# Kernel optimization log

Hardware: AMD Instinct MI355X
Metric: run time of the kernel (lower is better)

The kernel has to match this reference:

```python
import jax, jax.numpy as jnp
import numpy as np

B, E, S = 8, 128, 4096


def setup_inputs() -> dict:
    key = jax.random.key(0)
    ks = jax.random.split(key, 7)
    sc = 1.0 / np.sqrt(E)
    return {
        "x": jax.random.normal(ks[0], (B, E, S), dtype=jnp.float32),
        "Wq": jax.random.normal(ks[1], (E, E), dtype=jnp.float32) * sc,
        "bq": jax.random.normal(ks[2], (E,), dtype=jnp.float32) * 0.01,
        "Wk": jax.random.normal(ks[3], (E, E), dtype=jnp.float32) * sc,
        "bk": jax.random.normal(ks[4], (E,), dtype=jnp.float32) * 0.01,
        "Wv": jax.random.normal(ks[5], (E, E), dtype=jnp.float32) * sc,
        "bv": jax.random.normal(ks[6], (E,), dtype=jnp.float32) * 0.01,
    }


def reference(x, Wq, bq, Wk, bk, Wv, bv):
    # x: [B, E, S]; Conv1d(k=1) == per-position linear over channels.
    # Project then move to [B, S, E] (matches .permute(0, 2, 1)).
    Q = jnp.einsum('bes,fe->bsf', x, Wq) + bq  # [B, S, E]
    K = jnp.einsum('bes,fe->bsf', x, Wk) + bk
    V = jnp.einsum('bes,fe->bsf', x, Wv) + bv
    scale = jnp.sqrt(jnp.asarray(float(x.shape[1]), dtype=jnp.float32))
    attn = jnp.einsum('bqe,bke->bqk', Q, K) / scale  # [B, S, S]
    attn = jax.nn.softmax(attn, axis=2)
    out = jnp.einsum('bqk,bke->bqe', attn, V)  # [B, S, E]
    return out.transpose(0, 2, 1)  # [B, E, S]
```

## Files before the change

kernel.cpp:

```cpp
#include <hip/hip_runtime.h>
#include <math.h>

#define NB 8
#define NE 128
#define NS 4096
#define CSCALE 0.12751743f

typedef short s8v __attribute__((ext_vector_type(8)));
typedef float f4v __attribute__((ext_vector_type(4)));
typedef float f16v __attribute__((ext_vector_type(16)));
typedef unsigned int u32;
typedef unsigned int u2v __attribute__((ext_vector_type(2)));
typedef __attribute__((address_space(1))) const u32* gp1_t;
typedef __attribute__((address_space(3))) u32* lp3_t;

__device__ __forceinline__ ushort f2bf(float f) {
  union { float f; unsigned u; } v; v.f = f;
  unsigned r = v.u + 0x7fffu + ((v.u >> 16) & 1u);
  return (ushort)(r >> 16);
}
__device__ __forceinline__ float bf2f(ushort h) {
  union { unsigned u; float f; } v; v.u = ((unsigned)h) << 16; return v.f;
}
__device__ __forceinline__ void gload_lds16(const void* g, void* l) {
  __builtin_amdgcn_global_load_lds((gp1_t)g, (lp3_t)l, 16, 0, 0);
}
__device__ __forceinline__ u32 cvtpk(float lo, float hi) {
  u32 r;
  asm("v_cvt_pk_bf16_f32 %0, %1, %2" : "=v"(r) : "v"(lo), "v"(hi));
  return r;
}
__device__ __forceinline__ void split8(const float* __restrict__ p, float scale,
                                       s8v& hi, s8v& lo) {
  union { s8v v; ushort u[8]; } H, L;
  #pragma unroll
  for (int i = 0; i < 8; ++i) {
    float v = p[i] * scale;
    ushort h = f2bf(v);
    H.u[i] = h;
    L.u[i] = f2bf(v - bf2f(h));
  }
  hi = H.v; lo = L.v;
}

__global__ __launch_bounds__(256, 2) void proj_gemm(
    const float* __restrict__ x,
    const float* __restrict__ Wq, const float* __restrict__ bq,
    const float* __restrict__ Wk, const float* __restrict__ bk,
    const float* __restrict__ Wv, const float* __restrict__ bv,
    ushort* __restrict__ Qn, ushort* __restrict__ Kn, ushort* __restrict__ Vt)
{
  const int tid = threadIdx.x;
  const int wv = tid >> 6, lane = tid & 63;
  const int g = lane >> 4, c = lane & 15;
  const int bid = blockIdx.x;
  const int b = bid & 7;
  const int s0 = (bid >> 3) * 64;
  const float* xb = x + (size_t)b * NE * NS;

  __shared__ __align__(16) ushort xh[64][136], xl[64][136];

  {
    const int ss = tid & 63, cq = tid >> 6;
    #pragma unroll
    for (int p = 0; p < 4; ++p) {
      const int ch = p * 4 + cq;
      union { s8v v; ushort u[8]; } H, L;
      #pragma unroll
      for (int i = 0; i < 8; ++i) {
        float v = xb[(size_t)(ch * 8 + i) * NS + s0 + ss];
        ushort hi = f2bf(v);
        H.u[i] = hi;
        L.u[i] = f2bf(v - bf2f(hi));
      }
      *(s8v*)&xh[ss][ch * 8] = H.v;
      *(s8v*)&xl[ss][ch * 8] = L.v;
    }
  }
  __syncthreads();

  f4v aq[2][4], ak[2][4], av[2][4];
  #pragma unroll
  for (int i = 0; i < 2; ++i)
    #pragma unroll
    for (int j = 0; j < 4; ++j) {
      aq[i][j] = (f4v){0.f,0.f,0.f,0.f};
      ak[i][j] = (f4v){0.f,0.f,0.f,0.f};
      av[i][j] = (f4v){0.f,0.f,0.f,0.f};
    }

  #pragma unroll
  for (int ks = 0; ks < 4; ++ks) {
    s8v xbh[4], xbl[4];
    #pragma unroll
    for (int st = 0; st < 4; ++st) {
      xbh[st] = *(const s8v*)&xh[st * 16 + c][ks * 32 + g * 8];
      xbl[st] = *(const s8v*)&xl[st * 16 + c][ks * 32 + g * 8];
    }
    #pragma unroll
    for (int ftl = 0; ftl < 2; ++ftl) {
      const int f0 = (wv * 2 + ftl) * 16;
      const size_t wo = (size_t)(f0 + c) * NE + ks * 32 + g * 8;
      s8v qh, ql, kh, kl, vh, vl;
      split8(Wq + wo, CSCALE, qh, ql);
      split8(Wk + wo, 1.0f,   kh, kl);
      split8(Wv + wo, 1.0f,   vh, vl);
      #pragma unroll
      for (int st = 0; st < 4; ++st) {
        aq[ftl][st] = __builtin_amdgcn_mfma_f32_16x16x32_bf16(xbh[st], qh, aq[ftl][st], 0, 0, 0);
        aq[ftl][st] = __builtin_amdgcn_mfma_f32_16x16x32_bf16(xbl[st], qh, aq[ftl][st], 0, 0, 0);
        aq[ftl][st] = __builtin_amdgcn_mfma_f32_16x16x32_bf16(xbh[st], ql, aq[ftl][st], 0, 0, 0);
        av[ftl][st] = __builtin_amdgcn_mfma_f32_16x16x32_bf16(vh, xbh[st], av[ftl][st], 0, 0, 0);
        av[ftl][st] = __builtin_amdgcn_mfma_f32_16x16x32_bf16(vh, xbl[st], av[ftl][st], 0, 0, 0);
        av[ftl][st] = __builtin_amdgcn_mfma_f32_16x16x32_bf16(vl, xbh[st], av[ftl][st], 0, 0, 0);
        ak[ftl][st] = __builtin_amdgcn_mfma_f32_16x16x32_bf16(xbh[st], kh, ak[ftl][st], 0, 0, 0);
        ak[ftl][st] = __builtin_amdgcn_mfma_f32_16x16x32_bf16(xbl[st], kh, ak[ftl][st], 0, 0, 0);
        ak[ftl][st] = __builtin_amdgcn_mfma_f32_16x16x32_bf16(xbh[st], kl, ak[ftl][st], 0, 0, 0);
      }
    }
  }

  ushort* Qnb = Qn + (size_t)b * NS * NE;
  ushort* Knb = Kn + (size_t)b * NS * NE;
  ushort* Vtb = Vt + (size_t)b * NE * NS;
  #pragma unroll
  for (int ftl = 0; ftl < 2; ++ftl) {
    const int f0 = (wv * 2 + ftl) * 16;
    #pragma unroll
    for (int r = 0; r < 4; ++r) {
      const int f = f0 + 4 * g + r;
      const float bvv = bv[f];
      #pragma unroll
      for (int st = 0; st < 4; ++st)
        Vtb[(size_t)f * NS + s0 + st * 16 + c] = f2bf(av[ftl][st][r] + bvv);
    }
    const float bqv = bq[f0 + c] * CSCALE;
    const float bkv = bk[f0 + c];
    #pragma unroll
    for (int st = 0; st < 4; ++st)
      #pragma unroll
      for (int r = 0; r < 4; ++r) {
        const size_t ro = (size_t)(s0 + st * 16 + 4 * g + r) * NE + f0 + c;
        Qnb[ro] = f2bf(aq[ftl][st][r] + bqv);
        Knb[ro] = f2bf(ak[ftl][st][r] + bkv);
      }
  }
}

__global__ __launch_bounds__(256) void attn_kernel(
    const ushort* __restrict__ Qn, const ushort* __restrict__ Kn,
    const ushort* __restrict__ Vt, float* __restrict__ out)
{
  const int tid = threadIdx.x;
  const int wv = tid >> 6, lane = tid & 63;
  const int h = lane >> 5, q5 = lane & 31;
  const int bid = blockIdx.x;
  const int b = bid & 7;
  const int qw = (bid >> 3) * 128 + wv * 32;

  const ushort* Qb = Qn + (size_t)b * NS * NE;
  const char*   Kb = (const char*)(Kn + (size_t)b * NS * NE);
  const char*   Vb = (const char*)(Vt + (size_t)b * NE * NS);

  __shared__ __align__(16) char ldsK[2][16384];
  __shared__ __align__(16) char ldsV[2][16384];

  s8v qf[8];
  #pragma unroll
  for (int dc = 0; dc < 8; ++dc)
    qf[dc] = *(const s8v*)(Qb + (size_t)(qw + q5) * NE + dc * 16 + h * 8);

  auto stage = [&](int buf, int kt) {
    const char* Ksrc = Kb + (size_t)kt * (64 * 256);
    #pragma unroll
    for (int p = 0; p < 4; ++p) {
      const int off = wv * 4096 + p * 1024;
      const int lo = off + lane * 16;
      const int row = lo >> 8;
      gload_lds16(Ksrc + (lo ^ ((row & 7) << 4)), &ldsK[buf][off]);
    }
    #pragma unroll
    for (int p = 0; p < 4; ++p) {
      const int off = wv * 4096 + p * 1024;
      const int lo = off + lane * 16;
      const int row = lo >> 7;
      const int inner = (lo & 127) ^ ((row & 7) << 4);
      gload_lds16(Vb + (size_t)row * (NS * 2) + kt * 128 + inner, &ldsV[buf][off]);
    }
  };

  f16v o[4];
  #pragma unroll
  for (int dt = 0; dt < 4; ++dt)
    o[dt] = (f16v){0,0,0,0,0,0,0,0,0,0,0,0,0,0,0,0};
  float lsum = 0.f;

  stage(0, 0);
  asm volatile("s_waitcnt vmcnt(0)" ::: "memory");
  __syncthreads();

  #pragma unroll 1
  for (int kt = 0; kt < NS / 64; ++kt) {
    const int cur = kt & 1;
    if (kt + 1 < NS / 64) stage(cur ^ 1, kt + 1);
    const char* bK = ldsK[cur];
    const char* bV = ldsV[cur];

    #pragma unroll
    for (int kc = 0; kc < 2; ++kc) {
      f16v s = (f16v){0,0,0,0,0,0,0,0,0,0,0,0,0,0,0,0};
      #pragma unroll
      for (int dc = 0; dc < 8; ++dc) {
        s8v kf = *(const s8v*)(bK + (kc * 32 + q5) * 256 + ((dc * 32 + h * 16) ^ ((q5 & 7) << 4)));
        s = __builtin_amdgcn_mfma_f32_32x32x16_bf16(kf, qf[dc], s, 0, 0, 0);
      }
      float p[16];
      #pragma unroll
      for (int r = 0; r < 16; ++r) {
        p[r] = __builtin_amdgcn_exp2f(s[r]);
        lsum += p[r];
      }
      #pragma unroll
      for (int ksl = 0; ksl < 2; ++ksl) {
        const int r0 = ksl * 8;
        u32 A = cvtpk(p[r0 + 0], p[r0 + 1]);
        u32 B = cvtpk(p[r0 + 4], p[r0 + 5]);
        u32 C = cvtpk(p[r0 + 2], p[r0 + 3]);
        u32 D = cvtpk(p[r0 + 6], p[r0 + 7]);
        u2v rAB = __builtin_amdgcn_permlane32_swap(A, B, false, false);
        u2v rCD = __builtin_amdgcn_permlane32_swap(C, D, false, false);
        union { s8v v; u32 w[4]; } P;
        P.w[0] = rAB[0]; P.w[1] = rCD[0]; P.w[2] = rAB[1]; P.w[3] = rCD[1];
        const int ks = kc * 2 + ksl;
        #pragma unroll
        for (int dt = 0; dt < 4; ++dt) {
          s8v vf = *(const s8v*)(bV + (dt * 32 + q5) * 128 + ((ks * 32 + h * 16) ^ ((q5 & 7) << 4)));
          o[dt] = __builtin_amdgcn_mfma_f32_32x32x16_bf16(vf, P.v, o[dt], 0, 0, 0);
        }
      }
    }
    asm volatile("s_waitcnt vmcnt(0)" ::: "memory");
    __syncthreads();
  }

  lsum += __shfl_xor(lsum, 32);
  const float rinv = 1.0f / lsum;
  float* ob = out + (size_t)b * NE * NS;
  #pragma unroll
  for (int dt = 0; dt < 4; ++dt)
    #pragma unroll
    for (int r = 0; r < 16; ++r) {
      const int e = dt * 32 + (r & 3) + 8 * (r >> 2) + 4 * h;
      ob[(size_t)e * NS + qw + q5] = o[dt][r] * rinv;
    }
}

extern "C" void kernel_launch(void* const* d_in, const int* in_sizes, int n_in,
                              void* d_out, int out_size, void* d_ws, size_t ws_size,
                              hipStream_t stream) {
  const float* x  = (const float*)d_in[0];
  const float* Wq = (const float*)d_in[1];
  const float* bq = (const float*)d_in[2];
  const float* Wk = (const float*)d_in[3];
  const float* bk = (const float*)d_in[4];
  const float* Wv = (const float*)d_in[5];
  const float* bv = (const float*)d_in[6];
  float* out = (float*)d_out;

  ushort* Qn = (ushort*)d_ws;
  ushort* Kn = Qn + (size_t)NB * NS * NE;
  ushort* Vt = Kn + (size_t)NB * NS * NE;

  proj_gemm<<<dim3(NS / 64 * NB), 256, 0, stream>>>(x, Wq, bq, Wk, bk, Wv, bv, Qn, Kn, Vt);
  attn_kernel<<<dim3(NS / 128 * NB), 256, 0, stream>>>(Qn, Kn, Vt, out);
}
```

Before: 118.0 us.

## Split KV range across wave pairs with two query tiles per wave

Each wave now handles two 32-row query tiles, so every K and V fragment read from LDS feeds two MFMAs. The four waves form two slices that each cover half of the key sequence with their own double-buffered LDS tiles. The partial outputs and row sums are then combined through LDS at the end. This halves LDS fragment reads per MFMA but doubles accumulator registers and LDS footprint (about 128KB), and adds a final cross-wave reduction; launch bounds now force one block per CU.

```diff
diff --git a/kernel.cpp b/kernel.cpp
--- a/kernel.cpp
+++ b/kernel.cpp
@@ -147,95 +147,111 @@
   }
 }
 
-__global__ __launch_bounds__(256) void attn_kernel(
+__global__ __launch_bounds__(256, 1) void attn_kernel(
     const ushort* __restrict__ Qn, const ushort* __restrict__ Kn,
     const ushort* __restrict__ Vt, float* __restrict__ out)
 {
   const int tid = threadIdx.x;
   const int wv = tid >> 6, lane = tid & 63;
   const int h = lane >> 5, q5 = lane & 31;
+  const int slice = wv >> 1;
+  const int ws = wv & 1;
   const int bid = blockIdx.x;
   const int b = bid & 7;
-  const int qw = (bid >> 3) * 128 + wv * 32;
+  const int qw = (bid >> 3) * 128 + ws * 64;
 
   const ushort* Qb = Qn + (size_t)b * NS * NE;
   const char*   Kb = (const char*)(Kn + (size_t)b * NS * NE);
   const char*   Vb = (const char*)(Vt + (size_t)b * NE * NS);
 
-  __shared__ __align__(16) char ldsK[2][16384];
-  __shared__ __align__(16) char ldsV[2][16384];
-
-  s8v qf[8];
-  #pragma unroll
-  for (int dc = 0; dc < 8; ++dc)
-    qf[dc] = *(const s8v*)(Qb + (size_t)(qw + q5) * NE + dc * 16 + h * 8);
-
-  auto stage = [&](int buf, int kt) {
+  __shared__ __align__(16) char ldsK[2][2][16384];
+  __shared__ __align__(16) char ldsV[2][2][16384];
+  __shared__ float lx[2][2][32];
+
+  s8v qf[2][8];
+  #pragma unroll
+  for (int u = 0; u < 2; ++u)
+    #pragma unroll
+    for (int dc = 0; dc < 8; ++dc)
+      qf[u][dc] = *(const s8v*)(Qb + (size_t)(qw + u * 32 + q5) * NE + dc * 16 + h * 8);
+
+  auto stage = [&](int buf, int t) {
+    const int kt = slice * 32 + t;
     const char* Ksrc = Kb + (size_t)kt * (64 * 256);
     #pragma unroll
-    for (int p = 0; p < 4; ++p) {
-      const int off = wv * 4096 + p * 1024;
+    for (int p = 0; p < 8; ++p) {
+      const int off = ws * 8192 + p * 1024;
       const int lo = off + lane * 16;
       const int row = lo >> 8;
-      gload_lds16(Ksrc + (lo ^ ((row & 7) << 4)), &ldsK[buf][off]);
-    }
-    #pragma unroll
-    for (int p = 0; p < 4; ++p) {
-      const int off = wv * 4096 + p * 1024;
+      gload_lds16(Ksrc + (lo ^ ((row & 15) << 4)), &ldsK[slice][buf][off]);
+    }
+    #pragma unroll
+    for (int p = 0; p < 8; ++p) {
+      const int off = ws * 8192 + p * 1024;
       const int lo = off + lane * 16;
       const int row = lo >> 7;
       const int inner = (lo & 127) ^ ((row & 7) << 4);
-      gload_lds16(Vb + (size_t)row * (NS * 2) + kt * 128 + inner, &ldsV[buf][off]);
+      gload_lds16(Vb + (size_t)row * (NS * 2) + kt * 128 + inner, &ldsV[slice][buf][off]);
     }
   };
 
-  f16v o[4];
-  #pragma unroll
-  for (int dt = 0; dt < 4; ++dt)
-    o[dt] = (f16v){0,0,0,0,0,0,0,0,0,0,0,0,0,0,0,0};
-  float lsum = 0.f;
+  auto makefrag = [&](const float* p, int r0) -> s8v {
+    u32 A = cvtpk(p[r0 + 0], p[r0 + 1]);
+    u32 B = cvtpk(p[r0 + 4], p[r0 + 5]);
+    u32 C = cvtpk(p[r0 + 2], p[r0 + 3]);
+    u32 D = cvtpk(p[r0 + 6], p[r0 + 7]);
+    u2v rAB = __builtin_amdgcn_permlane32_swap(A, B, false, false);
+    u2v rCD = __builtin_amdgcn_permlane32_swap(C, D, false, false);
+    union { s8v v; u32 w[4]; } P;
+    P.w[0] = rAB[0]; P.w[1] = rCD[0]; P.w[2] = rAB[1]; P.w[3] = rCD[1];
+    return P.v;
+  };
+
+  f16v oA[4], oB[4];
+  #pragma unroll
+  for (int dt = 0; dt < 4; ++dt) {
+    oA[dt] = (f16v){0,0,0,0,0,0,0,0,0,0,0,0,0,0,0,0};
+    oB[dt] = (f16v){0,0,0,0,0,0,0,0,0,0,0,0,0,0,0,0};
+  }
+  float lA = 0.f, lB = 0.f;
 
   stage(0, 0);
   asm volatile("s_waitcnt vmcnt(0)" ::: "memory");
   __syncthreads();
 
   #pragma unroll 1
-  for (int kt = 0; kt < NS / 64; ++kt) {
-    const int cur = kt & 1;
-    if (kt + 1 < NS / 64) stage(cur ^ 1, kt + 1);
-    const char* bK = ldsK[cur];
-    const char* bV = ldsV[cur];
+  for (int t = 0; t < 32; ++t) {
+    const int cur = t & 1;
+    if (t + 1 < 32) stage(cur ^ 1, t + 1);
+    const char* bK = ldsK[slice][cur];
+    const char* bV = ldsV[slice][cur];
 
     #pragma unroll
     for (int kc = 0; kc < 2; ++kc) {
-      f16v s = (f16v){0,0,0,0,0,0,0,0,0,0,0,0,0,0,0,0};
+      f16v sA = (f16v){0,0,0,0,0,0,0,0,0,0,0,0,0,0,0,0};
+      f16v sB = (f16v){0,0,0,0,0,0,0,0,0,0,0,0,0,0,0,0};
       #pragma unroll
       for (int dc = 0; dc < 8; ++dc) {
-        s8v kf = *(const s8v*)(bK + (kc * 32 + q5) * 256 + ((dc * 32 + h * 16) ^ ((q5 & 7) << 4)));
-        s = __builtin_amdgcn_mfma_f32_32x32x16_bf16(kf, qf[dc], s, 0, 0, 0);
-      }
-      float p[16];
+        s8v kf = *(const s8v*)(bK + (kc * 32 + q5) * 256 + ((dc * 32 + h * 16) ^ ((q5 & 15) << 4)));
+        sA = __builtin_amdgcn_mfma_f32_32x32x16_bf16(kf, qf[0][dc], sA, 0, 0, 0);
+        sB = __builtin_amdgcn_mfma_f32_32x32x16_bf16(kf, qf[1][dc], sB, 0, 0, 0);
+      }
+      float pA[16], pB[16];
       #pragma unroll
       for (int r = 0; r < 16; ++r) {
-        p[r] = __builtin_amdgcn_exp2f(s[r]);
-        lsum += p[r];
+        pA[r] = __builtin_amdgcn_exp2f(sA[r]); lA += pA[r];
+        pB[r] = __builtin_amdgcn_exp2f(sB[r]); lB += pB[r];
       }
       #pragma unroll
       for (int ksl = 0; ksl < 2; ++ksl) {
-        const int r0 = ksl * 8;
-        u32 A = cvtpk(p[r0 + 0], p[r0 + 1]);
-        u32 B = cvtpk(p[r0 + 4], p[r0 + 5]);
-        u32 C = cvtpk(p[r0 + 2], p[r0 + 3]);
-        u32 D = cvtpk(p[r0 + 6], p[r0 + 7]);
-        u2v rAB = __builtin_amdgcn_permlane32_swap(A, B, false, false);
-        u2v rCD = __builtin_amdgcn_permlane32_swap(C, D, false, false);
-        union { s8v v; u32 w[4]; } P;
-        P.w[0] = rAB[0]; P.w[1] = rCD[0]; P.w[2] = rAB[1]; P.w[3] = rCD[1];
+        s8v PA = makefrag(pA, ksl * 8);
+        s8v PB = makefrag(pB, ksl * 8);
         const int ks = kc * 2 + ksl;
         #pragma unroll
         for (int dt = 0; dt < 4; ++dt) {
           s8v vf = *(const s8v*)(bV + (dt * 32 + q5) * 128 + ((ks * 32 + h * 16) ^ ((q5 & 7) << 4)));
-          o[dt] = __builtin_amdgcn_mfma_f32_32x32x16_bf16(vf, P.v, o[dt], 0, 0, 0);
+          oA[dt] = __builtin_amdgcn_mfma_f32_32x32x16_bf16(vf, PA, oA[dt], 0, 0, 0);
+          oB[dt] = __builtin_amdgcn_mfma_f32_32x32x16_bf16(vf, PB, oB[dt], 0, 0, 0);
         }
       }
     }
@@ -243,21 +259,41 @@
     __syncthreads();
   }
 
-  lsum += __shfl_xor(lsum, 32);
-  const float rinv = 1.0f / lsum;
-  float* ob = out + (size_t)b * NE * NS;
-  #pragma unroll
-  for (int dt = 0; dt < 4; ++dt)
-    #pragma unroll
-    for (int r = 0; r < 16; ++r) {
-      const int e = dt * 32 + (r & 3) + 8 * (r >> 2) + 4 * h;
-      ob[(size_t)e * NS + qw + q5] = o[dt][r] * rinv;
-    }
+  lA += __shfl_xor(lA, 32);
+  lB += __shfl_xor(lB, 32);
+  float* cb = (float*)&ldsK[0][0][0];
+  if (slice == 1) {
+    #pragma unroll
+    for (int dt = 0; dt < 4; ++dt)
+      #pragma unroll
+      for (int r = 0; r < 16; ++r) {
+        cb[ws * 8192 + (dt * 16 + r) * 64 + lane]      = oA[dt][r];
+        cb[ws * 8192 + (64 + dt * 16 + r) * 64 + lane] = oB[dt][r];
+      }
+    if (h == 0) { lx[ws][0][q5] = lA; lx[ws][1][q5] = lB; }
+  }
+  __syncthreads();
+  if (slice == 0) {
+    const float rA = 1.0f / (lA + lx[ws][0][q5]);
+    const float rB = 1.0f / (lB + lx[ws][1][q5]);
+    float* ob = out + (size_t)b * NE * NS;
+    #pragma unroll
+    for (int dt = 0; dt < 4; ++dt)
+      #pragma unroll
+      for (int r = 0; r < 16; ++r) {
+        const int e = dt * 32 + (r & 3) + 8 * (r >> 2) + 4 * h;
+        ob[(size_t)e * NS + qw + q5] =
+            (oA[dt][r] + cb[ws * 8192 + (dt * 16 + r) * 64 + lane]) * rA;
+        ob[(size_t)e * NS + qw + 32 + q5] =
+            (oB[dt][r] + cb[ws * 8192 + (64 + dt * 16 + r) * 64 + lane]) * rB;
+      }
+  }
 }
 
 extern "C" void kernel_launch(void* const* d_in, const int* in_sizes, int n_in,
                               void* d_out, int out_size, void* d_ws, size_t ws_size,
                               hipStream_t stream) {
+  (void)in_sizes; (void)n_in; (void)out_size; (void)ws_size;
   const float* x  = (const float*)d_in[0];
   const float* Wq = (const float*)d_in[1];
   const float* bq = (const float*)d_in[2];
```

New measurement: 119.0 us. No clear change (+0.8%).

## Split key range across two wave groups per block and merge partial outputs

Applied to the files above, without the earlier changes.

The attention block grows to 512 threads: two slices of four waves each process half of the key sequence for the same 128 queries. Each slice keeps its own double-buffered K/V tiles in a 128KB LDS region, and the partial outputs and row sums are reduced through LDS at the end. The stage split (two waves load K, two load V), the wider K swizzle, the batched QK MFMAs with setprio hints and the explicit barriers aim for more waves in flight and better MFMA/exp overlap. In exchange, the 128KB LDS footprint may limit residency despite the launch bound of two blocks, and the final cross-slice reduction adds extra work.

```diff
diff --git a/kernel.cpp b/kernel.cpp
--- a/kernel.cpp
+++ b/kernel.cpp
@@ -147,46 +147,77 @@
   }
 }
 
-__global__ __launch_bounds__(256) void attn_kernel(
+__global__ __launch_bounds__(512, 2) void attn_kernel(
     const ushort* __restrict__ Qn, const ushort* __restrict__ Kn,
     const ushort* __restrict__ Vt, float* __restrict__ out)
 {
   const int tid = threadIdx.x;
-  const int wv = tid >> 6, lane = tid & 63;
+  const int w = tid >> 6, lane = tid & 63;
   const int h = lane >> 5, q5 = lane & 31;
+  const int slice = w >> 2;
+  const int sub = w & 3;
   const int bid = blockIdx.x;
   const int b = bid & 7;
-  const int qw = (bid >> 3) * 128 + wv * 32;
+  const int qw = (bid >> 3) * 128 + sub * 32;
 
   const ushort* Qb = Qn + (size_t)b * NS * NE;
   const char*   Kb = (const char*)(Kn + (size_t)b * NS * NE);
   const char*   Vb = (const char*)(Vt + (size_t)b * NE * NS);
 
-  __shared__ __align__(16) char ldsK[2][16384];
-  __shared__ __align__(16) char ldsV[2][16384];
+  __shared__ __align__(16) char lds[131072];
+  __shared__ float lx[2][4][32];
+
+  auto Kbuf = [&](int bf) -> char* { return lds + slice * 65536 + bf * 32768; };
+  auto Vbuf = [&](int bf) -> char* { return Kbuf(bf) + 16384; };
 
   s8v qf[8];
   #pragma unroll
   for (int dc = 0; dc < 8; ++dc)
     qf[dc] = *(const s8v*)(Qb + (size_t)(qw + q5) * NE + dc * 16 + h * 8);
 
-  auto stage = [&](int buf, int kt) {
-    const char* Ksrc = Kb + (size_t)kt * (64 * 256);
-    #pragma unroll
-    for (int p = 0; p < 4; ++p) {
-      const int off = wv * 4096 + p * 1024;
-      const int lo = off + lane * 16;
-      const int row = lo >> 8;
-      gload_lds16(Ksrc + (lo ^ ((row & 7) << 4)), &ldsK[buf][off]);
-    }
-    #pragma unroll
-    for (int p = 0; p < 4; ++p) {
-      const int off = wv * 4096 + p * 1024;
-      const int lo = off + lane * 16;
-      const int row = lo >> 7;
-      const int inner = (lo & 127) ^ ((row & 7) << 4);
-      gload_lds16(Vb + (size_t)row * (NS * 2) + kt * 128 + inner, &ldsV[buf][off]);
-    }
+  auto stage = [&](int bf, int t) {
+    const int kt = slice * 32 + t;
+    if (sub < 2) {
+      const char* Ksrc = Kb + (size_t)kt * (64 * 256);
+      char* dst = Kbuf(bf);
+      const int base = sub * 8192;
+      #pragma unroll
+      for (int p = 0; p < 8; ++p) {
+        const int off = base + p * 1024;
+        const int lo = off + lane * 16;
+        const int row = lo >> 8;
+        gload_lds16(Ksrc + (lo ^ ((row & 15) << 4)), dst + off);
+      }
+    } else {
+      char* dst = Vbuf(bf);
+      const int base = (sub - 2) * 8192;
+      #pragma unroll
+      for (int p = 0; p < 8; ++p) {
+        const int off = base + p * 1024;
+        const int lo = off + lane * 16;
+        const int row = lo >> 7;
+        const int inner = (lo & 127) ^ ((row & 7) << 4);
+        gload_lds16(Vb + (size_t)row * (NS * 2) + kt * 128 + inner, dst + off);
+      }
+    }
+  };
+
+  auto expfrag8 = [&](float a0, float a1, float a2, float a3,
+                      float a4, float a5, float a6, float a7, float& l) -> s8v {
+    float p0 = __builtin_amdgcn_exp2f(a0), p1 = __builtin_amdgcn_exp2f(a1);
+    float p2 = __builtin_amdgcn_exp2f(a2), p3 = __builtin_amdgcn_exp2f(a3);
+    float p4 = __builtin_amdgcn_exp2f(a4), p5 = __builtin_amdgcn_exp2f(a5);
+    float p6 = __builtin_amdgcn_exp2f(a6), p7 = __builtin_amdgcn_exp2f(a7);
+    l += ((p0 + p1) + (p2 + p3)) + ((p4 + p5) + (p6 + p7));
+    u32 A = cvtpk(p0, p1);
+    u32 B = cvtpk(p4, p5);
+    u32 C = cvtpk(p2, p3);
+    u32 D = cvtpk(p6, p7);
+    u2v rAB = __builtin_amdgcn_permlane32_swap(A, B, false, false);
+    u2v rCD = __builtin_amdgcn_permlane32_swap(C, D, false, false);
+    union { s8v v; u32 wd[4]; } P;
+    P.wd[0] = rAB[0]; P.wd[1] = rCD[0]; P.wd[2] = rAB[1]; P.wd[3] = rCD[1];
+    return P.v;
   };
 
   f16v o[4];
@@ -197,67 +228,84 @@
 
   stage(0, 0);
   asm volatile("s_waitcnt vmcnt(0)" ::: "memory");
+  __builtin_amdgcn_sched_barrier(0);
+  __builtin_amdgcn_s_barrier();
+
+  #pragma unroll 1
+  for (int t = 0; t < 32; ++t) {
+    const int cur = t & 1;
+    if (t + 1 < 32) stage(cur ^ 1, t + 1);
+    const char* bK = Kbuf(cur);
+    const char* bV = Vbuf(cur);
+
+    f16v s0 = (f16v){0,0,0,0,0,0,0,0,0,0,0,0,0,0,0,0};
+    f16v s1 = (f16v){0,0,0,0,0,0,0,0,0,0,0,0,0,0,0,0};
+    __builtin_amdgcn_s_setprio(1);
+    #pragma unroll
+    for (int dc = 0; dc < 8; ++dc) {
+      s8v kf0 = *(const s8v*)(bK + (q5) * 256      + ((dc * 32 + h * 16) ^ ((q5 & 15) << 4)));
+      s8v kf1 = *(const s8v*)(bK + (32 + q5) * 256 + ((dc * 32 + h * 16) ^ ((q5 & 15) << 4)));
+      s0 = __builtin_amdgcn_mfma_f32_32x32x16_bf16(kf0, qf[dc], s0, 0, 0, 0);
+      s1 = __builtin_amdgcn_mfma_f32_32x32x16_bf16(kf1, qf[dc], s1, 0, 0, 0);
+    }
+    __builtin_amdgcn_s_setprio(0);
+
+    #pragma unroll
+    for (int ks = 0; ks < 4; ++ks) {
+      s8v P;
+      if (ks == 0)      P = expfrag8(s0[0], s0[1], s0[2], s0[3], s0[4], s0[5], s0[6], s0[7], lsum);
+      else if (ks == 1) P = expfrag8(s0[8], s0[9], s0[10], s0[11], s0[12], s0[13], s0[14], s0[15], lsum);
+      else if (ks == 2) P = expfrag8(s1[0], s1[1], s1[2], s1[3], s1[4], s1[5], s1[6], s1[7], lsum);
+      else              P = expfrag8(s1[8], s1[9], s1[10], s1[11], s1[12], s1[13], s1[14], s1[15], lsum);
+      __builtin_amdgcn_s_setprio(1);
+      #pragma unroll
+      for (int dt = 0; dt < 4; ++dt) {
+        s8v vf = *(const s8v*)(bV + (dt * 32 + q5) * 128 +
+                               ((ks * 32 + h * 16) ^ ((q5 & 7) << 4)));
+        o[dt] = __builtin_amdgcn_mfma_f32_32x32x16_bf16(vf, P, o[dt], 0, 0, 0);
+      }
+      __builtin_amdgcn_s_setprio(0);
+    }
+
+    asm volatile("s_waitcnt lgkmcnt(0)" ::: "memory");
+    __builtin_amdgcn_sched_barrier(0);
+    asm volatile("s_waitcnt vmcnt(0)" ::: "memory");
+    __builtin_amdgcn_sched_barrier(0);
+    __builtin_amdgcn_s_barrier();
+  }
+
+  lsum += __shfl_xor(lsum, 32);
+  if (h == 0) lx[slice][sub][q5] = lsum;
+  float* cb = (float*)lds;
   __syncthreads();
-
-  #pragma unroll 1
-  for (int kt = 0; kt < NS / 64; ++kt) {
-    const int cur = kt & 1;
-    if (kt + 1 < NS / 64) stage(cur ^ 1, kt + 1);
-    const char* bK = ldsK[cur];
-    const char* bV = ldsV[cur];
-
-    #pragma unroll
-    for (int kc = 0; kc < 2; ++kc) {
-      f16v s = (f16v){0,0,0,0,0,0,0,0,0,0,0,0,0,0,0,0};
-      #pragma unroll
-      for (int dc = 0; dc < 8; ++dc) {
-        s8v kf = *(const s8v*)(bK + (kc * 32 + q5) * 256 + ((dc * 32 + h * 16) ^ ((q5 & 7) << 4)));
-        s = __builtin_amdgcn_mfma_f32_32x32x16_bf16(kf, qf[dc], s, 0, 0, 0);
-      }
-      float p[16];
+  if (slice == 1) {
+    #pragma unroll
+    for (int dt = 0; dt < 4; ++dt)
       #pragma unroll
       for (int r = 0; r < 16; ++r) {
-        p[r] = __builtin_amdgcn_exp2f(s[r]);
-        lsum += p[r];
-      }
-      #pragma unroll
-      for (int ksl = 0; ksl < 2; ++ksl) {
-        const int r0 = ksl * 8;
-        u32 A = cvtpk(p[r0 + 0], p[r0 + 1]);
-        u32 B = cvtpk(p[r0 + 4], p[r0 + 5]);
-        u32 C = cvtpk(p[r0 + 2], p[r0 + 3]);
-        u32 D = cvtpk(p[r0 + 6], p[r0 + 7]);
-        u2v rAB = __builtin_amdgcn_permlane32_swap(A, B, false, false);
-        u2v rCD = __builtin_amdgcn_permlane32_swap(C, D, false, false);
-        union { s8v v; u32 w[4]; } P;
-        P.w[0] = rAB[0]; P.w[1] = rCD[0]; P.w[2] = rAB[1]; P.w[3] = rCD[1];
-        const int ks = kc * 2 + ksl;
-        #pragma unroll
-        for (int dt = 0; dt < 4; ++dt) {
-          s8v vf = *(const s8v*)(bV + (dt * 32 + q5) * 128 + ((ks * 32 + h * 16) ^ ((q5 & 7) << 4)));
-          o[dt] = __builtin_amdgcn_mfma_f32_32x32x16_bf16(vf, P.v, o[dt], 0, 0, 0);
-        }
-      }
-    }
-    asm volatile("s_waitcnt vmcnt(0)" ::: "memory");
-    __syncthreads();
-  }
-
-  lsum += __shfl_xor(lsum, 32);
-  const float rinv = 1.0f / lsum;
-  float* ob = out + (size_t)b * NE * NS;
-  #pragma unroll
-  for (int dt = 0; dt < 4; ++dt)
-    #pragma unroll
-    for (int r = 0; r < 16; ++r) {
-      const int e = dt * 32 + (r & 3) + 8 * (r >> 2) + 4 * h;
-      ob[(size_t)e * NS + qw + q5] = o[dt][r] * rinv;
-    }
+        const int e = dt * 32 + (r & 3) + 8 * (r >> 2) + 4 * h;
+        cb[sub * 4096 + e * 32 + q5] = o[dt][r];
+      }
+  }
+  __syncthreads();
+  if (slice == 0) {
+    const float rinv = 1.0f / (lx[0][sub][q5] + lx[1][sub][q5]);
+    float* ob = out + (size_t)b * NE * NS;
+    #pragma unroll
+    for (int dt = 0; dt < 4; ++dt)
+      #pragma unroll
+      for (int r = 0; r < 16; ++r) {
+        const int e = dt * 32 + (r & 3) + 8 * (r >> 2) + 4 * h;
+        ob[(size_t)e * NS + qw + q5] =
+            (o[dt][r] + cb[sub * 4096 + e * 32 + q5]) * rinv;
+      }
+  }
 }
 
 extern "C" void kernel_launch(void* const* d_in, const int* in_sizes, int n_in,
                               void* d_out, int out_size, void* d_ws, size_t ws_size,
                               hipStream_t stream) {
+  (void)in_sizes; (void)n_in; (void)out_size; (void)ws_size;
   const float* x  = (const float*)d_in[0];
   const float* Wq = (const float*)d_in[1];
   const float* bq = (const float*)d_in[2];
@@ -272,5 +320,5 @@
   ushort* Vt = Kn + (size_t)NB * NS * NE;
 
   proj_gemm<<<dim3(NS / 64 * NB), 256, 0, stream>>>(x, Wq, bq, Wk, bk, Wv, bv, Qn, Kn, Vt);
-  attn_kernel<<<dim3(NS / 128 * NB), 256, 0, stream>>>(Qn, Kn, Vt, out);
-}
+  attn_kernel<<<dim3(NS / 128 * NB), 512, 0, stream>>>(Qn, Kn, Vt, out);
+}
```

New measurement: 101.9 us. 1.16x faster.
